# Kernel tuning notes

Measured on AMD Instinct MI355X. Metric: run time of the kernel, lower is better.

## Reference

```python
import jax, jax.numpy as jnp
import numpy as np

N_NODES = 50000
N_EDGES = 800000
IN_CH = 128
HEADS = 4
OUT_CH = 32


def setup_inputs() -> dict:
    key = jax.random.key(0)
    k1, k2, k3, k4 = jax.random.split(key, 4)
    x = jax.random.normal(k1, (N_NODES, IN_CH), dtype=jnp.float32)
    edge_index = jax.random.randint(k2, (2, N_EDGES), 0, N_NODES, dtype=jnp.int64)
    # nn.Linear weight [out, in] with xavier-uniform init
    limW = float(np.sqrt(6.0 / (IN_CH + HEADS * OUT_CH)))
    W = jax.random.uniform(k3, (HEADS * OUT_CH, IN_CH), minval=-limW, maxval=limW, dtype=jnp.float32)
    lima = float(np.sqrt(6.0 / (HEADS + 2 * OUT_CH)))
    att = jax.random.uniform(k4, (HEADS, 2 * OUT_CH), minval=-lima, maxval=lima, dtype=jnp.float32)
    bias = jnp.zeros((HEADS * OUT_CH,), dtype=jnp.float32)
    return {"x": x, "edge_index": edge_index, "W": W, "att": att, "bias": bias}


def reference(x, edge_index, W, att, bias):
    n = x.shape[0]
    heads, two_c = att.shape
    out_ch = two_c // 2
    loop = jnp.arange(n, dtype=edge_index.dtype)
    src = jnp.concatenate([edge_index[0], loop])  # [E+n]
    dst = jnp.concatenate([edge_index[1], loop])  # [E+n]
    h = (x @ W.T).reshape(n, heads, out_ch)       # [n, H, C]
    h_src = h[src]                                # [E+n, H, C]
    h_dst = h[dst]                                # [E+n, H, C]
    # e = sum over channels of att applied to [h_src || h_dst]
    e = (jnp.einsum('ehc,hc->eh', h_src, att[:, :out_ch])
         + jnp.einsum('ehc,hc->eh', h_dst, att[:, out_ch:]))  # [E+n, H]
    e = jax.nn.leaky_relu(e, negative_slope=0.2)
    # segment softmax over incoming edges per dst node
    e_max = jax.ops.segment_max(e, dst, num_segments=n)        # [n, H]
    alpha = jnp.exp(e - e_max[dst])                            # [E+n, H]
    a_sum = jax.ops.segment_sum(alpha, dst, num_segments=n)    # [n, H]
    alpha = alpha / jnp.maximum(a_sum[dst], 1e-10)
    weighted = h_src * alpha[..., None]                        # [E+n, H, C]
    out = jax.ops.segment_sum(weighted, dst, num_segments=n)   # [n, H, C]
    out = out.reshape(n, heads * out_ch)                       # concat=True
    return out + bias
```

## Files before the change

### kernel.cpp

```cpp
#include <hip/hip_runtime.h>
#include <hip/hip_bf16.h>
#include <math.h>

#define N_NODES 50000
#define N_EDGES 800000
#define IN_CH   128
#define HEADS   4
#define OUT_CH  32
#define HC      128
#define WROWS   136

#define CB_SHIFT 6
#define CB_NODES 64
#define N_CB     782
#define NBK      128
#define EPB      (N_EDGES / NBK)
#define PCAP     28
#define ND_CAP   48

#define NG_TOT   782

typedef __attribute__((ext_vector_type(8))) short short8;
typedef __attribute__((ext_vector_type(8))) unsigned short ushort8;
typedef __attribute__((ext_vector_type(4))) float floatx4;

__device__ __forceinline__ short f2bf(float f) {
    __hip_bfloat16 h = __float2bfloat16(f);
    return *reinterpret_cast<short*>(&h);
}

__device__ __forceinline__ void gemm_role(
    short* __restrict__ Wlds, int node_base,
    const float* __restrict__ x, const float* __restrict__ W,
    const float* __restrict__ att, __hip_bfloat16* __restrict__ hbuf,
    float* __restrict__ asrc, float* __restrict__ adst) {

    const int tid  = threadIdx.x;
    const int wave = tid >> 6;
    const int lane = tid & 63;
    const int col  = lane & 15;
    const int q    = lane >> 4;

    {
        int row  = tid >> 1;
        int half = tid & 1;
        const float4* Wr = (const float4*)(W + row * IN_CH + half * 64);
        short* dp = Wlds + row * WROWS + half * 64;
#pragma unroll
        for (int i = 0; i < 16; ++i) {
            float4 v = Wr[i];
            ushort4 p;
            p.x = (unsigned short)f2bf(v.x);
            p.y = (unsigned short)f2bf(v.y);
            p.z = (unsigned short)f2bf(v.z);
            p.w = (unsigned short)f2bf(v.w);
            *(ushort4*)(dp + i * 4) = p;
        }
    }

    float attS[8], attD[8];
#pragma unroll
    for (int t = 0; t < 8; ++t) {
        int base = (t >> 1) * 64 + (t & 1) * 16 + col;
        attS[t] = att[base];
        attD[t] = att[base + 32];
    }

    __syncthreads();

    const int node0 = node_base + wave * 16;
    const int m  = node0 + col;
    const int mc = min(m, N_NODES - 1);

    floatx4 acc[8];
#pragma unroll
    for (int t = 0; t < 8; ++t) acc[t] = (floatx4){0.f, 0.f, 0.f, 0.f};

#pragma unroll
    for (int ks = 0; ks < 4; ++ks) {
        const float4* xp = (const float4*)(x + (size_t)mc * IN_CH + ks * 32 + q * 8);
        float4 v0 = xp[0];
        float4 v1 = xp[1];
        short8 af;
        af[0] = f2bf(v0.x); af[1] = f2bf(v0.y); af[2] = f2bf(v0.z); af[3] = f2bf(v0.w);
        af[4] = f2bf(v1.x); af[5] = f2bf(v1.y); af[6] = f2bf(v1.z); af[7] = f2bf(v1.w);
#pragma unroll
        for (int t = 0; t < 8; ++t) {
            const short8 bf = *(const short8*)(Wlds + (t * 16 + col) * WROWS + ks * 32 + q * 8);
            acc[t] = __builtin_amdgcn_mfma_f32_16x16x32_bf16(af, bf, acc[t], 0, 0, 0);
        }
    }

#pragma unroll
    for (int r = 0; r < 4; ++r) {
        const int node = node0 + q * 4 + r;
        const bool valid = node < N_NODES;
        float hs[4] = {0.f, 0.f, 0.f, 0.f};
        float hd[4] = {0.f, 0.f, 0.f, 0.f};
#pragma unroll
        for (int t = 0; t < 8; ++t) {
            float v = acc[t][r];
            if (valid) hbuf[(size_t)node * HC + t * 16 + col] = __float2bfloat16(v);
            hs[t >> 1] = fmaf(v, attS[t], hs[t >> 1]);
            hd[t >> 1] = fmaf(v, attD[t], hd[t >> 1]);
        }
#pragma unroll
        for (int off = 8; off; off >>= 1) {
#pragma unroll
            for (int h = 0; h < 4; ++h) {
                hs[h] += __shfl_down(hs[h], off, 16);
                hd[h] += __shfl_down(hd[h], off, 16);
            }
        }
        if (col == 0 && valid) {
#pragma unroll
            for (int h = 0; h < 4; ++h) {
                asrc[node * HEADS + h] = hs[h];
                adst[node * HEADS + h] = hd[h];
            }
        }
    }
}

__global__ __launch_bounds__(256) void k1_fused(
    const int* __restrict__ src, const int* __restrict__ dst,
    unsigned* __restrict__ priv, int* __restrict__ cnt2t,
    const float* __restrict__ x, const float* __restrict__ W,
    const float* __restrict__ att, __hip_bfloat16* __restrict__ hbuf,
    float* __restrict__ asrc, float* __restrict__ adst) {

    __shared__ short smem[128 * WROWS];
    const int tid = threadIdx.x;

    if (blockIdx.x < NBK) {
        int* lcnt = (int*)smem;
        const int blk = blockIdx.x;
        for (int i = tid; i < N_CB; i += 256) lcnt[i] = 0;
        __syncthreads();

        const int e0 = blk * EPB;
        for (int e = e0 + tid; e < e0 + EPB; e += 256) {
            int s = src[e];
            int d = dst[e];
            int cb = d >> CB_SHIFT;
            int pos = atomicAdd(&lcnt[cb], 1);
            if (pos < PCAP)
                priv[((size_t)cb * NBK + blk) * PCAP + pos] =
                    ((unsigned)(d & (CB_NODES - 1)) << 16) | (unsigned)s;
        }
        __syncthreads();
        for (int i = tid; i < N_CB; i += 256)
            cnt2t[i * NBK + blk] = min(lcnt[i], PCAP);
        return;
    }

    gemm_role(smem, (blockIdx.x - NBK) * 64, x, W, att, hbuf, asrc, adst);
}

__device__ __forceinline__ float edge_w(float t) {
    t = fmaxf(t, 0.2f * t);
    return __expf(t);
}

__device__ __forceinline__ void agg_one(
    int node, int cnt, const unsigned short* __restrict__ p,
    const unsigned* __restrict__ hb, const float* __restrict__ asrc,
    const float* __restrict__ adst, float2 bv,
    float* __restrict__ out, int lane, int h) {

    const float ad = adst[node * HEADS + h];

    unsigned us = hb[node * 64 + lane];
    float wS = edge_w(asrc[node * HEADS + h] + ad);
    float ds = wS;
    float ax = wS * __uint_as_float(us << 16);
    float ay = wS * __uint_as_float(us & 0xffff0000u);

    int e = 0;
    for (; e + 7 < cnt; e += 8) {
        ushort8 sv = *(const ushort8*)(p + e);
        int s0 = sv[0], s1 = sv[1], s2 = sv[2], s3 = sv[3];
        int s4 = sv[4], s5 = sv[5], s6 = sv[6], s7 = sv[7];
        unsigned u0 = hb[s0 * 64 + lane];
        unsigned u1 = hb[s1 * 64 + lane];
        unsigned u2 = hb[s2 * 64 + lane];
        unsigned u3 = hb[s3 * 64 + lane];
        unsigned u4 = hb[s4 * 64 + lane];
        unsigned u5 = hb[s5 * 64 + lane];
        unsigned u6 = hb[s6 * 64 + lane];
        unsigned u7 = hb[s7 * 64 + lane];
        float w0 = edge_w(asrc[s0 * HEADS + h] + ad);
        float w1 = edge_w(asrc[s1 * HEADS + h] + ad);
        float w2 = edge_w(asrc[s2 * HEADS + h] + ad);
        float w3 = edge_w(asrc[s3 * HEADS + h] + ad);
        float w4 = edge_w(asrc[s4 * HEADS + h] + ad);
        float w5 = edge_w(asrc[s5 * HEADS + h] + ad);
        float w6 = edge_w(asrc[s6 * HEADS + h] + ad);
        float w7 = edge_w(asrc[s7 * HEADS + h] + ad);
        ds += ((w0 + w1) + (w2 + w3)) + ((w4 + w5) + (w6 + w7));
        ax = fmaf(w0, __uint_as_float(u0 << 16), ax);
        ay = fmaf(w0, __uint_as_float(u0 & 0xffff0000u), ay);
        ax = fmaf(w1, __uint_as_float(u1 << 16), ax);
        ay = fmaf(w1, __uint_as_float(u1 & 0xffff0000u), ay);
        ax = fmaf(w2, __uint_as_float(u2 << 16), ax);
        ay = fmaf(w2, __uint_as_float(u2 & 0xffff0000u), ay);
        ax = fmaf(w3, __uint_as_float(u3 << 16), ax);
        ay = fmaf(w3, __uint_as_float(u3 & 0xffff0000u), ay);
        ax = fmaf(w4, __uint_as_float(u4 << 16), ax);
        ay = fmaf(w4, __uint_as_float(u4 & 0xffff0000u), ay);
        ax = fmaf(w5, __uint_as_float(u5 << 16), ax);
        ay = fmaf(w5, __uint_as_float(u5 & 0xffff0000u), ay);
        ax = fmaf(w6, __uint_as_float(u6 << 16), ax);
        ay = fmaf(w6, __uint_as_float(u6 & 0xffff0000u), ay);
        ax = fmaf(w7, __uint_as_float(u7 << 16), ax);
        ay = fmaf(w7, __uint_as_float(u7 & 0xffff0000u), ay);
    }
    for (; e + 3 < cnt; e += 4) {
        int s0 = p[e], s1 = p[e + 1], s2 = p[e + 2], s3 = p[e + 3];
        unsigned u0 = hb[s0 * 64 + lane];
        unsigned u1 = hb[s1 * 64 + lane];
        unsigned u2 = hb[s2 * 64 + lane];
        unsigned u3 = hb[s3 * 64 + lane];
        float w0 = edge_w(asrc[s0 * HEADS + h] + ad);
        float w1 = edge_w(asrc[s1 * HEADS + h] + ad);
        float w2 = edge_w(asrc[s2 * HEADS + h] + ad);
        float w3 = edge_w(asrc[s3 * HEADS + h] + ad);
        ds += (w0 + w1) + (w2 + w3);
        ax = fmaf(w0, __uint_as_float(u0 << 16), ax);
        ay = fmaf(w0, __uint_as_float(u0 & 0xffff0000u), ay);
        ax = fmaf(w1, __uint_as_float(u1 << 16), ax);
        ay = fmaf(w1, __uint_as_float(u1 & 0xffff0000u), ay);
        ax = fmaf(w2, __uint_as_float(u2 << 16), ax);
        ay = fmaf(w2, __uint_as_float(u2 & 0xffff0000u), ay);
        ax = fmaf(w3, __uint_as_float(u3 << 16), ax);
        ay = fmaf(w3, __uint_as_float(u3 & 0xffff0000u), ay);
    }
    for (; e < cnt; ++e) {
        int s0 = p[e];
        unsigned u0 = hb[s0 * 64 + lane];
        float w0 = edge_w(asrc[s0 * HEADS + h] + ad);
        ds += w0;
        ax = fmaf(w0, __uint_as_float(u0 << 16), ax);
        ay = fmaf(w0, __uint_as_float(u0 & 0xffff0000u), ay);
    }

    float inv = 1.0f / fmaxf(ds, 1e-10f);
    float2 o;
    o.x = ax * inv + bv.x;
    o.y = ay * inv + bv.y;
    *(float2*)(out + (size_t)node * HC + lane * 2) = o;
}

__global__ __launch_bounds__(1024) void k2_binagg(
    const int* __restrict__ cnt2t, const unsigned* __restrict__ priv,
    const unsigned* __restrict__ hb, const float* __restrict__ asrc,
    const float* __restrict__ adst, const float* __restrict__ bias,
    float* __restrict__ out) {

    __shared__ unsigned short list[CB_NODES * ND_CAP];
    __shared__ int lcnt[CB_NODES];
    __shared__ int lcnt2[NBK];

    const int b   = blockIdx.x;
    const int tid = threadIdx.x;

    if (tid < CB_NODES) lcnt[tid] = 0;
    if (tid < NBK) lcnt2[tid] = cnt2t[b * NBK + tid];
    __syncthreads();

    const unsigned* p = priv + (size_t)b * (NBK * PCAP);
    for (int idx = tid; idx < NBK * PCAP; idx += 1024) {
        int blk = (idx * 4682) >> 17;
        int j   = idx - blk * PCAP;
        if (j < lcnt2[blk]) {
            unsigned ent = p[idx];
            int dl   = ent >> 16;
            int slot = atomicAdd(&lcnt[dl], 1);
            if (slot < ND_CAP)
                list[dl * ND_CAP + slot] = (unsigned short)(ent & 0xFFFFu);
        }
    }
    __syncthreads();

    const int wv   = tid >> 6;
    const int lane = tid & 63;
    const int h    = lane >> 4;
    const float2 bv = *(const float2*)(bias + lane * 2);

#pragma unroll 1
    for (int rr = 0; rr < 4; ++rr) {
        const int dl   = (wv << 2) + rr;
        const int node = (b << CB_SHIFT) + dl;
        if (node >= N_NODES) break;
        const int cnt = min(lcnt[dl], ND_CAP);
        agg_one(node, cnt, &list[dl * ND_CAP],
                hb, asrc, adst, bv, out, lane, h);
    }
}

extern "C" void kernel_launch(void* const* d_in, const int* in_sizes, int n_in,
                              void* d_out, int out_size, void* d_ws, size_t ws_size,
                              hipStream_t stream) {
    const float* x    = (const float*)d_in[0];
    const int*   ei   = (const int*)d_in[1];
    const float* W    = (const float*)d_in[2];
    const float* att  = (const float*)d_in[3];
    const float* bias = (const float*)d_in[4];
    float* out = (float*)d_out;

    const int* src = ei;
    const int* dst = ei + N_EDGES;

    char* ws = (char*)d_ws;
    __hip_bfloat16* hbuf = (__hip_bfloat16*)ws;
    float*    asrc = (float*)(ws + 12800000);
    float*    adst = (float*)(ws + 13600000);
    unsigned* priv = (unsigned*)(ws + 14400000);
    int*      cnt2 = (int*)(ws + 25610752);

    k1_fused<<<NBK + NG_TOT, 256, 0, stream>>>(src, dst, priv, cnt2,
                                               x, W, att, hbuf, asrc, adst);
    k2_binagg<<<N_CB, 1024, 0, stream>>>(cnt2, priv, (const unsigned*)hbuf,
                                         asrc, adst, bias, out);
}
```

Before: 149.2 us.

## Replace two-level binned edge lists with direct per-node global atomic lists

Drops the two-level binning scheme, where blocks wrote private per-chunk buckets that the aggregation kernel re-sorted in LDS. Each edge now does a global atomicAdd on a per-destination counter and writes its source index straight into a fixed-capacity per-node list. The aggregation kernel becomes one wave per node, and a small zeroing kernel is added. This removes the LDS regroup pass and the private staging buffer, at the cost of 800k contended global atomics, scattered 2-byte writes and an extra launch.

```diff
diff --git a/kernel.cpp b/kernel.cpp
--- a/kernel.cpp
+++ b/kernel.cpp
@@ -10,12 +10,8 @@
 #define HC      128
 #define WROWS   136
 
-#define CB_SHIFT 6
-#define CB_NODES 64
-#define N_CB     782
-#define NBK      128
+#define NBK      256
 #define EPB      (N_EDGES / NBK)
-#define PCAP     28
 #define ND_CAP   48
 
 #define NG_TOT   782
@@ -27,6 +23,11 @@
 __device__ __forceinline__ short f2bf(float f) {
     __hip_bfloat16 h = __float2bfloat16(f);
     return *reinterpret_cast<short*>(&h);
+}
+
+__global__ __launch_bounds__(1024) void k0_zero(int* __restrict__ ncnt) {
+    int i = blockIdx.x * 1024 + threadIdx.x;
+    if (i < N_NODES) ncnt[i] = 0;
 }
 
 __device__ __forceinline__ void gemm_role(
@@ -124,7 +125,7 @@
 
 __global__ __launch_bounds__(256) void k1_fused(
     const int* __restrict__ src, const int* __restrict__ dst,
-    unsigned* __restrict__ priv, int* __restrict__ cnt2t,
+    int* __restrict__ ncnt, unsigned short* __restrict__ lists,
     const float* __restrict__ x, const float* __restrict__ W,
     const float* __restrict__ att, __hip_bfloat16* __restrict__ hbuf,
     float* __restrict__ asrc, float* __restrict__ adst) {
@@ -133,24 +134,31 @@
     const int tid = threadIdx.x;
 
     if (blockIdx.x < NBK) {
-        int* lcnt = (int*)smem;
         const int blk = blockIdx.x;
-        for (int i = tid; i < N_CB; i += 256) lcnt[i] = 0;
-        __syncthreads();
-
         const int e0 = blk * EPB;
-        for (int e = e0 + tid; e < e0 + EPB; e += 256) {
+        const int eN = e0 + EPB;
+        int e = e0 + tid;
+#pragma unroll 1
+        for (; e + 768 < eN; e += 1024) {
+            int s0 = src[e],       d0 = dst[e];
+            int s1 = src[e + 256], d1 = dst[e + 256];
+            int s2 = src[e + 512], d2 = dst[e + 512];
+            int s3 = src[e + 768], d3 = dst[e + 768];
+            int p0 = atomicAdd(&ncnt[d0], 1);
+            int p1 = atomicAdd(&ncnt[d1], 1);
+            int p2 = atomicAdd(&ncnt[d2], 1);
+            int p3 = atomicAdd(&ncnt[d3], 1);
+            if (p0 < ND_CAP) lists[(size_t)d0 * ND_CAP + p0] = (unsigned short)s0;
+            if (p1 < ND_CAP) lists[(size_t)d1 * ND_CAP + p1] = (unsigned short)s1;
+            if (p2 < ND_CAP) lists[(size_t)d2 * ND_CAP + p2] = (unsigned short)s2;
+            if (p3 < ND_CAP) lists[(size_t)d3 * ND_CAP + p3] = (unsigned short)s3;
+        }
+        for (; e < eN; e += 256) {
             int s = src[e];
             int d = dst[e];
-            int cb = d >> CB_SHIFT;
-            int pos = atomicAdd(&lcnt[cb], 1);
-            if (pos < PCAP)
-                priv[((size_t)cb * NBK + blk) * PCAP + pos] =
-                    ((unsigned)(d & (CB_NODES - 1)) << 16) | (unsigned)s;
-        }
-        __syncthreads();
-        for (int i = tid; i < N_CB; i += 256)
-            cnt2t[i * NBK + blk] = min(lcnt[i], PCAP);
+            int pos = atomicAdd(&ncnt[d], 1);
+            if (pos < ND_CAP) lists[(size_t)d * ND_CAP + pos] = (unsigned short)s;
+        }
         return;
     }
 
@@ -162,11 +170,19 @@
     return __expf(t);
 }
 
-__device__ __forceinline__ void agg_one(
-    int node, int cnt, const unsigned short* __restrict__ p,
+__global__ __launch_bounds__(256) void k2_agg(
+    const int* __restrict__ ncnt, const unsigned short* __restrict__ lists,
     const unsigned* __restrict__ hb, const float* __restrict__ asrc,
-    const float* __restrict__ adst, float2 bv,
-    float* __restrict__ out, int lane, int h) {
+    const float* __restrict__ adst, const float* __restrict__ bias,
+    float* __restrict__ out) {
+
+    const int node = __builtin_amdgcn_readfirstlane(blockIdx.x * 4 + (threadIdx.x >> 6));
+    if (node >= N_NODES) return;
+    const int lane = threadIdx.x & 63;
+    const int h    = lane >> 4;
+
+    const int cnt = min(ncnt[node], ND_CAP);
+    const unsigned short* p = lists + (size_t)node * ND_CAP;
 
     const float ad = adst[node * HEADS + h];
 
@@ -245,57 +261,11 @@
     }
 
     float inv = 1.0f / fmaxf(ds, 1e-10f);
+    float2 b = *(const float2*)(bias + lane * 2);
     float2 o;
-    o.x = ax * inv + bv.x;
-    o.y = ay * inv + bv.y;
+    o.x = ax * inv + b.x;
+    o.y = ay * inv + b.y;
     *(float2*)(out + (size_t)node * HC + lane * 2) = o;
-}
-
-__global__ __launch_bounds__(1024) void k2_binagg(
-    const int* __restrict__ cnt2t, const unsigned* __restrict__ priv,
-    const unsigned* __restrict__ hb, const float* __restrict__ asrc,
-    const float* __restrict__ adst, const float* __restrict__ bias,
-    float* __restrict__ out) {
-
-    __shared__ unsigned short list[CB_NODES * ND_CAP];
-    __shared__ int lcnt[CB_NODES];
-    __shared__ int lcnt2[NBK];
-
-    const int b   = blockIdx.x;
-    const int tid = threadIdx.x;
-
-    if (tid < CB_NODES) lcnt[tid] = 0;
-    if (tid < NBK) lcnt2[tid] = cnt2t[b * NBK + tid];
-    __syncthreads();
-
-    const unsigned* p = priv + (size_t)b * (NBK * PCAP);
-    for (int idx = tid; idx < NBK * PCAP; idx += 1024) {
-        int blk = (idx * 4682) >> 17;
-        int j   = idx - blk * PCAP;
-        if (j < lcnt2[blk]) {
-            unsigned ent = p[idx];
-            int dl   = ent >> 16;
-            int slot = atomicAdd(&lcnt[dl], 1);
-            if (slot < ND_CAP)
-                list[dl * ND_CAP + slot] = (unsigned short)(ent & 0xFFFFu);
-        }
-    }
-    __syncthreads();
-
-    const int wv   = tid >> 6;
-    const int lane = tid & 63;
-    const int h    = lane >> 4;
-    const float2 bv = *(const float2*)(bias + lane * 2);
-
-#pragma unroll 1
-    for (int rr = 0; rr < 4; ++rr) {
-        const int dl   = (wv << 2) + rr;
-        const int node = (b << CB_SHIFT) + dl;
-        if (node >= N_NODES) break;
-        const int cnt = min(lcnt[dl], ND_CAP);
-        agg_one(node, cnt, &list[dl * ND_CAP],
-                hb, asrc, adst, bv, out, lane, h);
-    }
 }
 
 extern "C" void kernel_launch(void* const* d_in, const int* in_sizes, int n_in,
@@ -313,13 +283,14 @@
 
     char* ws = (char*)d_ws;
     __hip_bfloat16* hbuf = (__hip_bfloat16*)ws;
-    float*    asrc = (float*)(ws + 12800000);
-    float*    adst = (float*)(ws + 13600000);
-    unsigned* priv = (unsigned*)(ws + 14400000);
-    int*      cnt2 = (int*)(ws + 25610752);
-
-    k1_fused<<<NBK + NG_TOT, 256, 0, stream>>>(src, dst, priv, cnt2,
+    float* asrc = (float*)(ws + 12800000);
+    float* adst = (float*)(ws + 13600000);
+    int*   ncnt = (int*)(ws + 14400000);
+    unsigned short* lists = (unsigned short*)(ws + 14600000);
+
+    k0_zero<<<(N_NODES + 1023) / 1024, 1024, 0, stream>>>(ncnt);
+    k1_fused<<<NBK + NG_TOT, 256, 0, stream>>>(src, dst, ncnt, lists,
                                                x, W, att, hbuf, asrc, adst);
-    k2_binagg<<<N_CB, 1024, 0, stream>>>(cnt2, priv, (const unsigned*)hbuf,
-                                         asrc, adst, bias, out);
-}
+    k2_agg<<<(N_NODES + 3) / 4, 256, 0, stream>>>(ncnt, lists, (const unsigned*)hbuf,
+                                                  asrc, adst, bias, out);
+}
```

New measurement: 166.7 us. +11.8%, slower.
